# Kernel optimization log

Hardware: AMD Instinct MI355X
Metric: run time of the kernel (lower is better)

## Reference

```python
import jax, jax.numpy as jnp
import numpy as np

WH, WW = 7, 7
N = WH * WW
DIM = 128
NH = 4
HD = DIM // NH
B_IMG, NW = 64, 64
B_ = B_IMG * NW

def _relative_position_index():
    ch = np.arange(WH)
    cw = np.arange(WW)
    coords = np.stack(np.meshgrid(ch, cw, indexing='ij'))  # (2, Wh, Ww)
    coords = coords.reshape(2, -1)  # (2, N)
    rel = coords[:, :, None] - coords[:, None, :]  # (2, N, N)
    rel = rel.transpose(1, 2, 0)  # (N, N, 2)
    rel[:, :, 0] += WH - 1
    rel[:, :, 1] += WW - 1
    rel[:, :, 0] *= 2 * WW - 1
    return jnp.asarray(rel.sum(-1), dtype=jnp.int32)  # (N, N)

REL_IDX = _relative_position_index()

def setup_inputs() -> dict:
    key = jax.random.key(0)
    k1, k2, k3, k4, k5 = jax.random.split(key, 5)
    return {
        'x': jax.random.normal(k1, (B_, N, DIM), dtype=jnp.float32),
        'mask': jax.random.normal(k2, (NW, N, N), dtype=jnp.float32),
        'qkv_w': jax.random.normal(k3, (3 * DIM, DIM), dtype=jnp.float32) * 0.02,
        'qkv_b': jax.random.normal(k4, (3 * DIM,), dtype=jnp.float32) * 0.02,
        'rel_table': jax.random.normal(k5, ((2 * WH - 1) * (2 * WW - 1), NH), dtype=jnp.float32) * 0.02,
    }

def reference(x, mask, qkv_w, qkv_b, rel_table):
    B_tot, n, c = x.shape
    scale = HD ** (-0.5)
    # qkv projection; torch split order is (nH, hD, qkv) innermost-to-outermost
    qkv = x @ qkv_w.T + qkv_b                      # (B_, N, 3C)
    qkv = qkv.reshape(B_tot, n, NH, HD, 3)
    q = jnp.transpose(qkv[..., 0], (0, 2, 1, 3))   # (B_, nH, N, hD)
    k = jnp.transpose(qkv[..., 1], (0, 2, 1, 3))
    v = jnp.transpose(qkv[..., 2], (0, 2, 1, 3))
    attn = jnp.einsum('bhnd,bhmd->bhnm', q, k) * scale  # (B_, nH, N, N)
    bias = jnp.transpose(rel_table[REL_IDX.reshape(-1)].reshape(n, n, NH), (2, 0, 1))
    attn = attn + bias[None]
    nW = mask.shape[0]
    attn = attn.reshape(B_tot // nW, nW, NH, n, n) + mask[None, :, None]
    attn = attn.reshape(B_tot, NH, n, n)
    attn = jax.nn.softmax(attn, axis=-1)
    out = jnp.einsum('bhnm,bhmd->bhnd', attn, v)   # (B_, nH, N, hD)
    return jnp.transpose(out, (0, 2, 1, 3)).reshape(B_tot, n, c)
```

## Files before the change

### kernel.cpp

```cpp
#include <hip/hip_runtime.h>


typedef short bf16x8 __attribute__((ext_vector_type(8)));
typedef float f32x4 __attribute__((ext_vector_type(4)));

#define DEVI __device__ __forceinline__

DEVI unsigned short f2b(float f) {
    unsigned u = __builtin_bit_cast(unsigned, f);
    u += 0x7fffu + ((u >> 16) & 1u);
    return (unsigned short)(u >> 16);
}

#define WS_BIAS_OFF 98304
#define WS_COMB_OFF 131072
#define COMB_ELEMS  802816u
#define WS_NEED     (131072u + COMB_ELEMS * 4u)

__global__ __launch_bounds__(256) void prep_kernel(
    const float* __restrict__ qkvw, const float* __restrict__ qkvb,
    const float* __restrict__ maskg, const float* __restrict__ relt,
    unsigned short* __restrict__ wb, float* __restrict__ bb,
    float* __restrict__ comb)
{
    const int g = blockIdx.x * 256 + threadIdx.x;
    if (g < 49152) {
        const int row = g >> 7, col = g & 127;
        const int s = row >> 7, r7 = row & 127, hh = r7 >> 5, d = r7 & 31;
        const int c = hh * 96 + d * 3 + s;
        const float mul = (s == 0) ? 0.17677669529663687f : 1.0f;
        wb[row * 128 + col] = f2b(qkvw[c * 128 + col] * mul);
    } else if (g < 49536) {
        const int row = g - 49152;
        const int s = row >> 7, r7 = row & 127, hh = r7 >> 5, d = r7 & 31;
        const int c = hh * 96 + d * 3 + s;
        const float mul = (s == 0) ? 0.17677669529663687f : 1.0f;
        bb[row] = qkvb[c] * mul;
    } else {
        const unsigned g2 = (unsigned)(g - 49536);
        if (g2 < COMB_ELEMS) {
            const int wh = g2 / 3136;
            const int rr = g2 - wh * 3136;
            const int m = rr >> 6, n = rr & 63;
            const int w = wh >> 2, hh = wh & 3;
            float v = -1e30f;
            if (n < 49) {
                const int md = m / 7, mm = m - md * 7;
                const int nd = n / 7, nm = n - nd * 7;
                const int ridx = (md - nd + 6) * 13 + (mm - nm + 6);
                v = maskg[w * 2401 + m * 49 + n] + relt[ridx * 4 + hh];
            }
            comb[g2] = v;
        }
    }
}

struct __align__(16) Smem {
    unsigned short qk[2][4][64][32];
    union {
        unsigned short xs[64][136];
        unsigned short vt[4][32][72];
    } b;
};

template <bool USE_WS>
__global__ __launch_bounds__(512, 6) void wattn_kernel(
    const float* __restrict__ xg, const unsigned short* __restrict__ wb,
    const float* __restrict__ bb, const float* __restrict__ comb,
    const float* __restrict__ maskg, const float* __restrict__ qkvw,
    const float* __restrict__ qkvb, const float* __restrict__ relt,
    float* __restrict__ outg)
{
    __shared__ Smem sm;
    const int tid  = threadIdx.x;
    const int lane = tid & 63;
    const int wv   = tid >> 6;
    const int h    = wv & 3;
    const int half = wv >> 2;
    const int lr   = lane & 15;
    const int lq   = lane >> 4;
    const int bI   = blockIdx.x;

    const float* xb = xg + (size_t)bI * 6272;
    #pragma unroll
    for (int it = 0; it < 4; ++it) {
        int i = it * 512 + tid;
        if (i < 1568) {
            float4 v = ((const float4*)xb)[i];
            int row = i >> 5, col = (i & 31) << 2;
            *(ushort4*)&sm.b.xs[row][col] =
                make_ushort4(f2b(v.x), f2b(v.y), f2b(v.z), f2b(v.w));
        }
    }
    if (tid < 480) {
        int idx = tid << 2;
        *(ushort4*)&sm.b.xs[49 + (idx >> 7)][idx & 127] = make_ushort4(0, 0, 0, 0);
    }
    __syncthreads();

    bf16x8 af[4][2];
    #pragma unroll
    for (int ks = 0; ks < 4; ++ks)
        #pragma unroll
        for (int mtl = 0; mtl < 2; ++mtl)
            af[ks][mtl] = *(const bf16x8*)&sm.b.xs[(half * 2 + mtl) * 16 + lr][ks * 32 + lq * 8];
    __syncthreads();

    if constexpr (USE_WS) {
        #pragma unroll
        for (int j = 0; j < 6; ++j) {
            const int s     = j >> 1;
            const int dhalf = j & 1;
            const int cp    = s * 128 + h * 32 + dhalf * 16 + lr;
            const int dd    = dhalf * 16 + lr;
            const float bc  = bb[cp];
            f32x4 acc[2];
            acc[0] = f32x4{0.f, 0.f, 0.f, 0.f};
            acc[1] = f32x4{0.f, 0.f, 0.f, 0.f};
            #pragma unroll
            for (int ks = 0; ks < 4; ++ks) {
                bf16x8 bf = *(const bf16x8*)&wb[cp * 128 + ks * 32 + lq * 8];
                #pragma unroll
                for (int mtl = 0; mtl < 2; ++mtl)
                    acc[mtl] = __builtin_amdgcn_mfma_f32_16x16x32_bf16(af[ks][mtl], bf, acc[mtl], 0, 0, 0);
            }
            #pragma unroll
            for (int mtl = 0; mtl < 2; ++mtl) {
                const int m0 = (half * 2 + mtl) * 16 + lq * 4;
                if (s == 2) {
                    *(ushort4*)&sm.b.vt[h][dd][m0] =
                        make_ushort4(f2b(acc[mtl][0] + bc), f2b(acc[mtl][1] + bc),
                                     f2b(acc[mtl][2] + bc), f2b(acc[mtl][3] + bc));
                } else {
                    #pragma unroll
                    for (int r = 0; r < 4; ++r)
                        sm.qk[s][h][m0 + r][dd] = f2b(acc[mtl][r] + bc);
                }
            }
        }
    } else {
        unsigned short* sbase = (unsigned short*)&sm;
        #pragma unroll
        for (int j = 0; j < 6; ++j) {
            const int c = (h * 6 + j) * 16 + lr;
            const float bc = qkvb[c];
            const int rem = j * 16 + lr;
            const int dd = rem / 3, s = rem % 3;
            const float mulv = (s == 0) ? 0.17677669529663687f : 1.0f;
            f32x4 acc[2];
            acc[0] = f32x4{0.f, 0.f, 0.f, 0.f};
            acc[1] = f32x4{0.f, 0.f, 0.f, 0.f};
            #pragma unroll
            for (int ks = 0; ks < 4; ++ks) {
                const float4* wp = (const float4*)(qkvw + c * 128 + ks * 32 + lq * 8);
                float4 w0 = wp[0], w1 = wp[1];
                bf16x8 t;
                t[0] = (short)f2b(w0.x); t[1] = (short)f2b(w0.y);
                t[2] = (short)f2b(w0.z); t[3] = (short)f2b(w0.w);
                t[4] = (short)f2b(w1.x); t[5] = (short)f2b(w1.y);
                t[6] = (short)f2b(w1.z); t[7] = (short)f2b(w1.w);
                #pragma unroll
                for (int mtl = 0; mtl < 2; ++mtl)
                    acc[mtl] = __builtin_amdgcn_mfma_f32_16x16x32_bf16(af[ks][mtl], t, acc[mtl], 0, 0, 0);
            }
            #pragma unroll
            for (int mtl = 0; mtl < 2; ++mtl)
                #pragma unroll
                for (int r = 0; r < 4; ++r) {
                    int m = (half * 2 + mtl) * 16 + lq * 4 + r;
                    int soff = (s == 2) ? (16384 + (h * 32 + dd) * 72 + m)
                                        : (s * 8192 + h * 2048 + m * 32 + dd);
                    sbase[soff] = f2b((acc[mtl][r] + bc) * mulv);
                }
        }
    }
    __syncthreads();

    bf16x8 kf[4];
    #pragma unroll
    for (int t = 0; t < 4; ++t)
        kf[t] = *(const bf16x8*)&sm.qk[1][h][t * 16 + lr][lq * 8];

    const float* cwh = comb + (size_t)((bI & 63) * 4 + h) * 3136;
    const float* mw  = maskg + (size_t)(bI & 63) * 2401;
    float* ob = outg + (size_t)bI * 6272;
    const int src0 = ((lq & 1) * 2) * 16 + lr;
    const int src1 = src0 + 16;
    const bool up  = (lq >= 2);

    #pragma unroll
    for (int bl = 0; bl < 2; ++bl) {
        const int mt = half * 2 + bl;
        const int m  = mt * 16 + lr;
        const int mi = m < 48 ? m : 48;

        f32x4 st[4];
        bf16x8 qf = *(const bf16x8*)&sm.qk[0][h][m][lq * 8];
        if constexpr (USE_WS) {
            const float* cr = cwh + mi * 64;
            f32x4 cc[4];
            #pragma unroll
            for (int a = 0; a < 4; ++a)
                cc[a] = *(const f32x4*)&cr[a * 16 + lq * 4];
            #pragma unroll
            for (int a = 0; a < 4; ++a)
                st[a] = __builtin_amdgcn_mfma_f32_16x16x32_bf16(kf[a], qf, cc[a], 0, 0, 0);
        } else {
            #pragma unroll
            for (int a = 0; a < 4; ++a) {
                f32x4 z = f32x4{0.f, 0.f, 0.f, 0.f};
                st[a] = __builtin_amdgcn_mfma_f32_16x16x32_bf16(kf[a], qf, z, 0, 0, 0);
            }
            const int md = mi / 7, mm = mi - md * 7;
            #pragma unroll
            for (int a = 0; a < 4; ++a)
                #pragma unroll
                for (int r = 0; r < 4; ++r) {
                    int n = a * 16 + lq * 4 + r;
                    int ni = n < 48 ? n : 48;
                    int nd = ni / 7, nm = ni - nd * 7;
                    int ridx = (md - nd + 6) * 13 + (mm - nm + 6);
                    float v = st[a][r] + relt[ridx * 4 + h] + mw[mi * 49 + ni];
                    st[a][r] = (n < 49) ? v : -1e30f;
                }
        }

        float mx = -3.4e38f;
        #pragma unroll
        for (int a = 0; a < 4; ++a)
            #pragma unroll
            for (int r = 0; r < 4; ++r) mx = fmaxf(mx, st[a][r]);
        mx = fmaxf(mx, __shfl_xor(mx, 16));
        mx = fmaxf(mx, __shfl_xor(mx, 32));
        float sum = 0.f;
        #pragma unroll
        for (int a = 0; a < 4; ++a)
            #pragma unroll
            for (int r = 0; r < 4; ++r) {
                float e = __expf(st[a][r] - mx);
                st[a][r] = e;
                sum += e;
            }
        sum += __shfl_xor(sum, 16);
        sum += __shfl_xor(sum, 32);
        const float inv = 1.f / sum;

        unsigned pk[4][2];
        #pragma unroll
        for (int a = 0; a < 4; ++a) {
            pk[a][0] = (unsigned)f2b(st[a][0] * inv) | ((unsigned)f2b(st[a][1] * inv) << 16);
            pk[a][1] = (unsigned)f2b(st[a][2] * inv) | ((unsigned)f2b(st[a][3] * inv) << 16);
        }

        f32x4 o[2];
        o[0] = f32x4{0.f, 0.f, 0.f, 0.f};
        o[1] = f32x4{0.f, 0.f, 0.f, 0.f};
        #pragma unroll
        for (int kt = 0; kt < 2; ++kt) {
            unsigned ea0 = (unsigned)__shfl((int)pk[2 * kt][0], src0);
            unsigned ea1 = (unsigned)__shfl((int)pk[2 * kt][1], src0);
            unsigned ea2 = (unsigned)__shfl((int)pk[2 * kt][0], src1);
            unsigned ea3 = (unsigned)__shfl((int)pk[2 * kt][1], src1);
            unsigned eb0 = (unsigned)__shfl((int)pk[2 * kt + 1][0], src0);
            unsigned eb1 = (unsigned)__shfl((int)pk[2 * kt + 1][1], src0);
            unsigned eb2 = (unsigned)__shfl((int)pk[2 * kt + 1][0], src1);
            unsigned eb3 = (unsigned)__shfl((int)pk[2 * kt + 1][1], src1);
            union { unsigned u[4]; bf16x8 v; } pu;
            pu.u[0] = up ? eb0 : ea0;
            pu.u[1] = up ? eb1 : ea1;
            pu.u[2] = up ? eb2 : ea2;
            pu.u[3] = up ? eb3 : ea3;
            #pragma unroll
            for (int dt = 0; dt < 2; ++dt) {
                bf16x8 vf = *(const bf16x8*)&sm.b.vt[h][dt * 16 + lr][kt * 32 + lq * 8];
                o[dt] = __builtin_amdgcn_mfma_f32_16x16x32_bf16(vf, pu.v, o[dt], 0, 0, 0);
            }
        }

        if (m < 49) {
            #pragma unroll
            for (int dt = 0; dt < 2; ++dt) {
                float4 v = make_float4(o[dt][0], o[dt][1], o[dt][2], o[dt][3]);
                *(float4*)&ob[m * 128 + h * 32 + dt * 16 + lq * 4] = v;
            }
        }
    }
}

extern "C" void kernel_launch(void* const* d_in, const int* in_sizes, int n_in,
                              void* d_out, int out_size, void* d_ws, size_t ws_size,
                              hipStream_t stream) {
    const float* x    = (const float*)d_in[0];
    const float* mask = (const float*)d_in[1];
    const float* qkvw = (const float*)d_in[2];
    const float* qkvb = (const float*)d_in[3];
    const float* relt = (const float*)d_in[4];
    float* out = (float*)d_out;

    if (d_ws != nullptr && ws_size >= (size_t)WS_NEED) {
        unsigned short* wbf = (unsigned short*)d_ws;
        float* bbf  = (float*)((char*)d_ws + WS_BIAS_OFF);
        float* comb = (float*)((char*)d_ws + WS_COMB_OFF);
        prep_kernel<<<3330, 256, 0, stream>>>(qkvw, qkvb, mask, relt, wbf, bbf, comb);
        wattn_kernel<true><<<4096, 512, 0, stream>>>(x, wbf, bbf, comb, mask, qkvw, qkvb, relt, out);
    } else {
        wattn_kernel<false><<<4096, 512, 0, stream>>>(x, nullptr, nullptr, nullptr, mask, qkvw, qkvb, relt, out);
    }
}
```

Measured before the change: 274.6 us.

## Keep Q in registers via transposed MFMA and shuffles, shrink LDS

```diff
diff --git a/kernel.cpp b/kernel.cpp
--- a/kernel.cpp
+++ b/kernel.cpp
@@ -10,6 +10,10 @@
     unsigned u = __builtin_bit_cast(unsigned, f);
     u += 0x7fffu + ((u >> 16) & 1u);
     return (unsigned short)(u >> 16);
+}
+
+DEVI unsigned pack2(float lo, float hi) {
+    return (unsigned)f2b(lo) | ((unsigned)f2b(hi) << 16);
 }
 
 #define WS_BIAS_OFF 98304
@@ -55,28 +59,24 @@
     }
 }
 
-struct __align__(16) Smem {
-    unsigned short qk[2][4][64][32];
+struct __align__(16) SmemWS {
+    unsigned short kk[4][64][32];
     union {
         unsigned short xs[64][136];
         unsigned short vt[4][32][72];
     } b;
 };
 
-template <bool USE_WS>
-__global__ __launch_bounds__(512, 6) void wattn_kernel(
+__global__ __launch_bounds__(512, 6) void wattn_ws(
     const float* __restrict__ xg, const unsigned short* __restrict__ wb,
     const float* __restrict__ bb, const float* __restrict__ comb,
-    const float* __restrict__ maskg, const float* __restrict__ qkvw,
-    const float* __restrict__ qkvb, const float* __restrict__ relt,
     float* __restrict__ outg)
 {
-    __shared__ Smem sm;
+    __shared__ SmemWS sm;
     const int tid  = threadIdx.x;
     const int lane = tid & 63;
-    const int wv   = tid >> 6;
-    const int h    = wv & 3;
-    const int half = wv >> 2;
+    const int h    = (tid >> 6) & 3;
+    const int half = tid >> 8;
     const int lr   = lane & 15;
     const int lq   = lane >> 4;
     const int bI   = blockIdx.x;
@@ -106,72 +106,102 @@
             af[ks][mtl] = *(const bf16x8*)&sm.b.xs[(half * 2 + mtl) * 16 + lr][ks * 32 + lq * 8];
     __syncthreads();
 
-    if constexpr (USE_WS) {
-        #pragma unroll
-        for (int j = 0; j < 6; ++j) {
-            const int s     = j >> 1;
-            const int dhalf = j & 1;
-            const int cp    = s * 128 + h * 32 + dhalf * 16 + lr;
-            const int dd    = dhalf * 16 + lr;
-            const float bc  = bb[cp];
-            f32x4 acc[2];
-            acc[0] = f32x4{0.f, 0.f, 0.f, 0.f};
-            acc[1] = f32x4{0.f, 0.f, 0.f, 0.f};
+    unsigned qfr[2][4];
+    {
+        f32x4 aq[2][2];
+        __builtin_amdgcn_s_setprio(1);
+        #pragma unroll
+        for (int dh = 0; dh < 2; ++dh) {
+            const int cp = h * 32 + dh * 16 + lr;
+            aq[dh][0] = f32x4{0.f, 0.f, 0.f, 0.f};
+            aq[dh][1] = f32x4{0.f, 0.f, 0.f, 0.f};
             #pragma unroll
             for (int ks = 0; ks < 4; ++ks) {
-                bf16x8 bf = *(const bf16x8*)&wb[cp * 128 + ks * 32 + lq * 8];
-                #pragma unroll
-                for (int mtl = 0; mtl < 2; ++mtl)
-                    acc[mtl] = __builtin_amdgcn_mfma_f32_16x16x32_bf16(af[ks][mtl], bf, acc[mtl], 0, 0, 0);
-            }
+                bf16x8 wf = *(const bf16x8*)&wb[cp * 128 + ks * 32 + lq * 8];
+                aq[dh][0] = __builtin_amdgcn_mfma_f32_16x16x32_bf16(wf, af[ks][0], aq[dh][0], 0, 0, 0);
+                aq[dh][1] = __builtin_amdgcn_mfma_f32_16x16x32_bf16(wf, af[ks][1], aq[dh][1], 0, 0, 0);
+            }
+        }
+        __builtin_amdgcn_s_setprio(0);
+        unsigned pq[2][2][2];
+        #pragma unroll
+        for (int dh = 0; dh < 2; ++dh) {
+            const float4 qb = *(const float4*)&bb[h * 32 + dh * 16 + lq * 4];
             #pragma unroll
             for (int mtl = 0; mtl < 2; ++mtl) {
-                const int m0 = (half * 2 + mtl) * 16 + lq * 4;
-                if (s == 2) {
-                    *(ushort4*)&sm.b.vt[h][dd][m0] =
-                        make_ushort4(f2b(acc[mtl][0] + bc), f2b(acc[mtl][1] + bc),
-                                     f2b(acc[mtl][2] + bc), f2b(acc[mtl][3] + bc));
-                } else {
-                    #pragma unroll
-                    for (int r = 0; r < 4; ++r)
-                        sm.qk[s][h][m0 + r][dd] = f2b(acc[mtl][r] + bc);
-                }
-            }
-        }
-    } else {
-        unsigned short* sbase = (unsigned short*)&sm;
-        #pragma unroll
-        for (int j = 0; j < 6; ++j) {
-            const int c = (h * 6 + j) * 16 + lr;
-            const float bc = qkvb[c];
-            const int rem = j * 16 + lr;
-            const int dd = rem / 3, s = rem % 3;
-            const float mulv = (s == 0) ? 0.17677669529663687f : 1.0f;
-            f32x4 acc[2];
-            acc[0] = f32x4{0.f, 0.f, 0.f, 0.f};
-            acc[1] = f32x4{0.f, 0.f, 0.f, 0.f};
-            #pragma unroll
-            for (int ks = 0; ks < 4; ++ks) {
-                const float4* wp = (const float4*)(qkvw + c * 128 + ks * 32 + lq * 8);
-                float4 w0 = wp[0], w1 = wp[1];
-                bf16x8 t;
-                t[0] = (short)f2b(w0.x); t[1] = (short)f2b(w0.y);
-                t[2] = (short)f2b(w0.z); t[3] = (short)f2b(w0.w);
-                t[4] = (short)f2b(w1.x); t[5] = (short)f2b(w1.y);
-                t[6] = (short)f2b(w1.z); t[7] = (short)f2b(w1.w);
-                #pragma unroll
-                for (int mtl = 0; mtl < 2; ++mtl)
-                    acc[mtl] = __builtin_amdgcn_mfma_f32_16x16x32_bf16(af[ks][mtl], t, acc[mtl], 0, 0, 0);
-            }
+                pq[dh][mtl][0] = pack2(aq[dh][mtl][0] + qb.x, aq[dh][mtl][1] + qb.y);
+                pq[dh][mtl][1] = pack2(aq[dh][mtl][2] + qb.z, aq[dh][mtl][3] + qb.w);
+            }
+        }
+        const int s0 = lr + ((lq & 1) * 2) * 16;
+        const int s1 = s0 + 16;
+        const bool hi = (lq >= 2);
+        #pragma unroll
+        for (int bl = 0; bl < 2; ++bl) {
+            unsigned a0 = (unsigned)__shfl((int)pq[0][bl][0], s0);
+            unsigned b0 = (unsigned)__shfl((int)pq[1][bl][0], s0);
+            unsigned a1 = (unsigned)__shfl((int)pq[0][bl][1], s0);
+            unsigned b1 = (unsigned)__shfl((int)pq[1][bl][1], s0);
+            unsigned a2 = (unsigned)__shfl((int)pq[0][bl][0], s1);
+            unsigned b2 = (unsigned)__shfl((int)pq[1][bl][0], s1);
+            unsigned a3 = (unsigned)__shfl((int)pq[0][bl][1], s1);
+            unsigned b3 = (unsigned)__shfl((int)pq[1][bl][1], s1);
+            qfr[bl][0] = hi ? b0 : a0;
+            qfr[bl][1] = hi ? b1 : a1;
+            qfr[bl][2] = hi ? b2 : a2;
+            qfr[bl][3] = hi ? b3 : a3;
+        }
+    }
+
+    #pragma unroll
+    for (int dh = 0; dh < 2; ++dh) {
+        const int cp = 128 + h * 32 + dh * 16 + lr;
+        const int dd = dh * 16 + lr;
+        const float bc = bb[cp];
+        f32x4 acc[2];
+        acc[0] = f32x4{0.f, 0.f, 0.f, 0.f};
+        acc[1] = f32x4{0.f, 0.f, 0.f, 0.f};
+        __builtin_amdgcn_s_setprio(1);
+        #pragma unroll
+        for (int ks = 0; ks < 4; ++ks) {
+            bf16x8 bf = *(const bf16x8*)&wb[cp * 128 + ks * 32 + lq * 8];
             #pragma unroll
             for (int mtl = 0; mtl < 2; ++mtl)
-                #pragma unroll
-                for (int r = 0; r < 4; ++r) {
-                    int m = (half * 2 + mtl) * 16 + lq * 4 + r;
-                    int soff = (s == 2) ? (16384 + (h * 32 + dd) * 72 + m)
-                                        : (s * 8192 + h * 2048 + m * 32 + dd);
-                    sbase[soff] = f2b((acc[mtl][r] + bc) * mulv);
-                }
+                acc[mtl] = __builtin_amdgcn_mfma_f32_16x16x32_bf16(af[ks][mtl], bf, acc[mtl], 0, 0, 0);
+        }
+        __builtin_amdgcn_s_setprio(0);
+        #pragma unroll
+        for (int mtl = 0; mtl < 2; ++mtl) {
+            const int m0 = (half * 2 + mtl) * 16 + lq * 4;
+            #pragma unroll
+            for (int r = 0; r < 4; ++r)
+                sm.kk[h][m0 + r][dd] = f2b(acc[mtl][r] + bc);
+        }
+    }
+
+    #pragma unroll
+    for (int dh = 0; dh < 2; ++dh) {
+        const int cp = 256 + h * 32 + dh * 16 + lr;
+        const int dd = dh * 16 + lr;
+        const float bc = bb[cp];
+        f32x4 acc[2];
+        acc[0] = f32x4{0.f, 0.f, 0.f, 0.f};
+        acc[1] = f32x4{0.f, 0.f, 0.f, 0.f};
+        __builtin_amdgcn_s_setprio(1);
+        #pragma unroll
+        for (int ks = 0; ks < 4; ++ks) {
+            bf16x8 bf = *(const bf16x8*)&wb[cp * 128 + ks * 32 + lq * 8];
+            #pragma unroll
+            for (int mtl = 0; mtl < 2; ++mtl)
+                acc[mtl] = __builtin_amdgcn_mfma_f32_16x16x32_bf16(af[ks][mtl], bf, acc[mtl], 0, 0, 0);
+        }
+        __builtin_amdgcn_s_setprio(0);
+        #pragma unroll
+        for (int mtl = 0; mtl < 2; ++mtl) {
+            const int m0 = (half * 2 + mtl) * 16 + lq * 4;
+            *(ushort4*)&sm.b.vt[h][dd][m0] =
+                make_ushort4(f2b(acc[mtl][0] + bc), f2b(acc[mtl][1] + bc),
+                             f2b(acc[mtl][2] + bc), f2b(acc[mtl][3] + bc));
         }
     }
     __syncthreads();
@@ -179,10 +209,9 @@
     bf16x8 kf[4];
     #pragma unroll
     for (int t = 0; t < 4; ++t)
-        kf[t] = *(const bf16x8*)&sm.qk[1][h][t * 16 + lr][lq * 8];
+        kf[t] = *(const bf16x8*)&sm.kk[h][t * 16 + lr][lq * 8];
 
     const float* cwh = comb + (size_t)((bI & 63) * 4 + h) * 3136;
-    const float* mw  = maskg + (size_t)(bI & 63) * 2401;
     float* ob = outg + (size_t)bI * 6272;
     const int src0 = ((lq & 1) * 2) * 16 + lr;
     const int src1 = src0 + 16;
@@ -194,36 +223,19 @@
         const int m  = mt * 16 + lr;
         const int mi = m < 48 ? m : 48;
 
+        union { unsigned u[4]; bf16x8 v; } qu;
+        qu.u[0] = qfr[bl][0]; qu.u[1] = qfr[bl][1];
+        qu.u[2] = qfr[bl][2]; qu.u[3] = qfr[bl][3];
+
+        const float* cr = cwh + mi * 64;
         f32x4 st[4];
-        bf16x8 qf = *(const bf16x8*)&sm.qk[0][h][m][lq * 8];
-        if constexpr (USE_WS) {
-            const float* cr = cwh + mi * 64;
-            f32x4 cc[4];
-            #pragma unroll
-            for (int a = 0; a < 4; ++a)
-                cc[a] = *(const f32x4*)&cr[a * 16 + lq * 4];
-            #pragma unroll
-            for (int a = 0; a < 4; ++a)
-                st[a] = __builtin_amdgcn_mfma_f32_16x16x32_bf16(kf[a], qf, cc[a], 0, 0, 0);
-        } else {
-            #pragma unroll
-            for (int a = 0; a < 4; ++a) {
-                f32x4 z = f32x4{0.f, 0.f, 0.f, 0.f};
-                st[a] = __builtin_amdgcn_mfma_f32_16x16x32_bf16(kf[a], qf, z, 0, 0, 0);
-            }
-            const int md = mi / 7, mm = mi - md * 7;
-            #pragma unroll
-            for (int a = 0; a < 4; ++a)
-                #pragma unroll
-                for (int r = 0; r < 4; ++r) {
-                    int n = a * 16 + lq * 4 + r;
-                    int ni = n < 48 ? n : 48;
-                    int nd = ni / 7, nm = ni - nd * 7;
-                    int ridx = (md - nd + 6) * 13 + (mm - nm + 6);
-                    float v = st[a][r] + relt[ridx * 4 + h] + mw[mi * 49 + ni];
-                    st[a][r] = (n < 49) ? v : -1e30f;
-                }
-        }
+        __builtin_amdgcn_s_setprio(1);
+        #pragma unroll
+        for (int a = 0; a < 4; ++a) {
+            f32x4 cc = *(const f32x4*)&cr[a * 16 + lq * 4];
+            st[a] = __builtin_amdgcn_mfma_f32_16x16x32_bf16(kf[a], qu.v, cc, 0, 0, 0);
+        }
+        __builtin_amdgcn_s_setprio(0);
 
         float mx = -3.4e38f;
         #pragma unroll
@@ -248,8 +260,8 @@
         unsigned pk[4][2];
         #pragma unroll
         for (int a = 0; a < 4; ++a) {
-            pk[a][0] = (unsigned)f2b(st[a][0] * inv) | ((unsigned)f2b(st[a][1] * inv) << 16);
-            pk[a][1] = (unsigned)f2b(st[a][2] * inv) | ((unsigned)f2b(st[a][3] * inv) << 16);
+            pk[a][0] = pack2(st[a][0] * inv, st[a][1] * inv);
+            pk[a][1] = pack2(st[a][2] * inv, st[a][3] * inv);
         }
 
         f32x4 o[2];
@@ -270,6 +282,191 @@
             pu.u[1] = up ? eb1 : ea1;
             pu.u[2] = up ? eb2 : ea2;
             pu.u[3] = up ? eb3 : ea3;
+            __builtin_amdgcn_s_setprio(1);
+            #pragma unroll
+            for (int dt = 0; dt < 2; ++dt) {
+                bf16x8 vf = *(const bf16x8*)&sm.b.vt[h][dt * 16 + lr][kt * 32 + lq * 8];
+                o[dt] = __builtin_amdgcn_mfma_f32_16x16x32_bf16(vf, pu.v, o[dt], 0, 0, 0);
+            }
+            __builtin_amdgcn_s_setprio(0);
+        }
+
+        if (m < 49) {
+            #pragma unroll
+            for (int dt = 0; dt < 2; ++dt) {
+                float4 v = make_float4(o[dt][0], o[dt][1], o[dt][2], o[dt][3]);
+                *(float4*)&ob[m * 128 + h * 32 + dt * 16 + lq * 4] = v;
+            }
+        }
+    }
+}
+
+struct __align__(16) SmemFB {
+    unsigned short qk[2][4][64][32];
+    union {
+        unsigned short xs[64][136];
+        unsigned short vt[4][32][72];
+    } b;
+};
+
+__global__ __launch_bounds__(512, 6) void wattn_fb(
+    const float* __restrict__ xg, const float* __restrict__ maskg,
+    const float* __restrict__ qkvw, const float* __restrict__ qkvb,
+    const float* __restrict__ relt, float* __restrict__ outg)
+{
+    __shared__ SmemFB sm;
+    const int tid  = threadIdx.x;
+    const int lane = tid & 63;
+    const int wv   = tid >> 6;
+    const int h    = wv & 3;
+    const int half = wv >> 2;
+    const int lr   = lane & 15;
+    const int lq   = lane >> 4;
+    const int bI   = blockIdx.x;
+
+    const float* xb = xg + (size_t)bI * 6272;
+    #pragma unroll
+    for (int it = 0; it < 4; ++it) {
+        int i = it * 512 + tid;
+        if (i < 1568) {
+            float4 v = ((const float4*)xb)[i];
+            int row = i >> 5, col = (i & 31) << 2;
+            *(ushort4*)&sm.b.xs[row][col] =
+                make_ushort4(f2b(v.x), f2b(v.y), f2b(v.z), f2b(v.w));
+        }
+    }
+    if (tid < 480) {
+        int idx = tid << 2;
+        *(ushort4*)&sm.b.xs[49 + (idx >> 7)][idx & 127] = make_ushort4(0, 0, 0, 0);
+    }
+    __syncthreads();
+
+    bf16x8 af[4][2];
+    #pragma unroll
+    for (int ks = 0; ks < 4; ++ks)
+        #pragma unroll
+        for (int mtl = 0; mtl < 2; ++mtl)
+            af[ks][mtl] = *(const bf16x8*)&sm.b.xs[(half * 2 + mtl) * 16 + lr][ks * 32 + lq * 8];
+    __syncthreads();
+
+    unsigned short* sbase = (unsigned short*)&sm;
+    #pragma unroll
+    for (int j = 0; j < 6; ++j) {
+        const int c = (h * 6 + j) * 16 + lr;
+        const float bc = qkvb[c];
+        const int rem = j * 16 + lr;
+        const int dd = rem / 3, s = rem % 3;
+        const float mulv = (s == 0) ? 0.17677669529663687f : 1.0f;
+        f32x4 acc[2];
+        acc[0] = f32x4{0.f, 0.f, 0.f, 0.f};
+        acc[1] = f32x4{0.f, 0.f, 0.f, 0.f};
+        #pragma unroll
+        for (int ks = 0; ks < 4; ++ks) {
+            const float4* wp = (const float4*)(qkvw + c * 128 + ks * 32 + lq * 8);
+            float4 w0 = wp[0], w1 = wp[1];
+            bf16x8 t;
+            t[0] = (short)f2b(w0.x); t[1] = (short)f2b(w0.y);
+            t[2] = (short)f2b(w0.z); t[3] = (short)f2b(w0.w);
+            t[4] = (short)f2b(w1.x); t[5] = (short)f2b(w1.y);
+            t[6] = (short)f2b(w1.z); t[7] = (short)f2b(w1.w);
+            #pragma unroll
+            for (int mtl = 0; mtl < 2; ++mtl)
+                acc[mtl] = __builtin_amdgcn_mfma_f32_16x16x32_bf16(af[ks][mtl], t, acc[mtl], 0, 0, 0);
+        }
+        #pragma unroll
+        for (int mtl = 0; mtl < 2; ++mtl)
+            #pragma unroll
+            for (int r = 0; r < 4; ++r) {
+                int m = (half * 2 + mtl) * 16 + lq * 4 + r;
+                int soff = (s == 2) ? (16384 + (h * 32 + dd) * 72 + m)
+                                    : (s * 8192 + h * 2048 + m * 32 + dd);
+                sbase[soff] = f2b((acc[mtl][r] + bc) * mulv);
+            }
+    }
+    __syncthreads();
+
+    bf16x8 kf[4];
+    #pragma unroll
+    for (int t = 0; t < 4; ++t)
+        kf[t] = *(const bf16x8*)&sm.qk[1][h][t * 16 + lr][lq * 8];
+
+    const float* mw = maskg + (size_t)(bI & 63) * 2401;
+    float* ob = outg + (size_t)bI * 6272;
+    const int src0 = ((lq & 1) * 2) * 16 + lr;
+    const int src1 = src0 + 16;
+    const bool up  = (lq >= 2);
+
+    #pragma unroll
+    for (int bl = 0; bl < 2; ++bl) {
+        const int mt = half * 2 + bl;
+        const int m  = mt * 16 + lr;
+        const int mi = m < 48 ? m : 48;
+
+        f32x4 st[4];
+        bf16x8 qf = *(const bf16x8*)&sm.qk[0][h][m][lq * 8];
+        #pragma unroll
+        for (int a = 0; a < 4; ++a) {
+            f32x4 z = f32x4{0.f, 0.f, 0.f, 0.f};
+            st[a] = __builtin_amdgcn_mfma_f32_16x16x32_bf16(kf[a], qf, z, 0, 0, 0);
+        }
+        const int md = mi / 7, mm = mi - md * 7;
+        #pragma unroll
+        for (int a = 0; a < 4; ++a)
+            #pragma unroll
+            for (int r = 0; r < 4; ++r) {
+                int n = a * 16 + lq * 4 + r;
+                int ni = n < 48 ? n : 48;
+                int nd = ni / 7, nm = ni - nd * 7;
+                int ridx = (md - nd + 6) * 13 + (mm - nm + 6);
+                float v = st[a][r] + relt[ridx * 4 + h] + mw[mi * 49 + ni];
+                st[a][r] = (n < 49) ? v : -1e30f;
+            }
+
+        float mx = -3.4e38f;
+        #pragma unroll
+        for (int a = 0; a < 4; ++a)
+            #pragma unroll
+            for (int r = 0; r < 4; ++r) mx = fmaxf(mx, st[a][r]);
+        mx = fmaxf(mx, __shfl_xor(mx, 16));
+        mx = fmaxf(mx, __shfl_xor(mx, 32));
+        float sum = 0.f;
+        #pragma unroll
+        for (int a = 0; a < 4; ++a)
+            #pragma unroll
+            for (int r = 0; r < 4; ++r) {
+                float e = __expf(st[a][r] - mx);
+                st[a][r] = e;
+                sum += e;
+            }
+        sum += __shfl_xor(sum, 16);
+        sum += __shfl_xor(sum, 32);
+        const float inv = 1.f / sum;
+
+        unsigned pk[4][2];
+        #pragma unroll
+        for (int a = 0; a < 4; ++a) {
+            pk[a][0] = pack2(st[a][0] * inv, st[a][1] * inv);
+            pk[a][1] = pack2(st[a][2] * inv, st[a][3] * inv);
+        }
+
+        f32x4 o[2];
+        o[0] = f32x4{0.f, 0.f, 0.f, 0.f};
+        o[1] = f32x4{0.f, 0.f, 0.f, 0.f};
+        #pragma unroll
+        for (int kt = 0; kt < 2; ++kt) {
+            unsigned ea0 = (unsigned)__shfl((int)pk[2 * kt][0], src0);
+            unsigned ea1 = (unsigned)__shfl((int)pk[2 * kt][1], src0);
+            unsigned ea2 = (unsigned)__shfl((int)pk[2 * kt][0], src1);
+            unsigned ea3 = (unsigned)__shfl((int)pk[2 * kt][1], src1);
+            unsigned eb0 = (unsigned)__shfl((int)pk[2 * kt + 1][0], src0);
+            unsigned eb1 = (unsigned)__shfl((int)pk[2 * kt + 1][1], src0);
+            unsigned eb2 = (unsigned)__shfl((int)pk[2 * kt + 1][0], src1);
+            unsigned eb3 = (unsigned)__shfl((int)pk[2 * kt + 1][1], src1);
+            union { unsigned u[4]; bf16x8 v; } pu;
+            pu.u[0] = up ? eb0 : ea0;
+            pu.u[1] = up ? eb1 : ea1;
+            pu.u[2] = up ? eb2 : ea2;
+            pu.u[3] = up ? eb3 : ea3;
             #pragma unroll
             for (int dt = 0; dt < 2; ++dt) {
                 bf16x8 vf = *(const bf16x8*)&sm.b.vt[h][dt * 16 + lr][kt * 32 + lq * 8];
@@ -302,8 +499,8 @@
         float* bbf  = (float*)((char*)d_ws + WS_BIAS_OFF);
         float* comb = (float*)((char*)d_ws + WS_COMB_OFF);
         prep_kernel<<<3330, 256, 0, stream>>>(qkvw, qkvb, mask, relt, wbf, bbf, comb);
-        wattn_kernel<true><<<4096, 512, 0, stream>>>(x, wbf, bbf, comb, mask, qkvw, qkvb, relt, out);
+        wattn_ws<<<4096, 512, 0, stream>>>(x, wbf, bbf, comb, out);
     } else {
-        wattn_kernel<false><<<4096, 512, 0, stream>>>(x, nullptr, nullptr, nullptr, mask, qkvw, qkvb, relt, out);
+        wattn_fb<<<4096, 512, 0, stream>>>(x, mask, qkvw, qkvb, relt, out);
     }
 }
```

Result: slower. 292.3 us (+6.5%).
